# Kernel optimization log

Hardware: AMD Instinct MI355X
Metric: run time of the kernel (lower is better)

## Reference

```python
import jax, jax.numpy as jnp
import numpy as np

B, IN_DIM, NUM_PROD, OUT_DIM = 65536, 1024, 2048, 2048

def setup_inputs() -> dict:
    key = jax.random.key(0)
    k1, k2, k3 = jax.random.split(key, 3)
    x = jax.random.normal(k1, (B, IN_DIM), dtype=jnp.float32)
    prod_indices = jax.random.randint(k2, (NUM_PROD, 2), 0, IN_DIM, dtype=jnp.int32)
    # prod_linear: nn.Linear(num_prod, out_dim, bias=False) -> weight [out_dim, num_prod]
    W_prod = jax.random.normal(k3, (OUT_DIM, NUM_PROD), dtype=jnp.float32) * 0.02
    return {"x": x, "prod_indices": prod_indices, "W_prod": W_prod}

def reference(x, prod_indices, W_prod):
    # calc_quads: for each k, x[..., i_k] * x[..., j_k]  (vectorized gather-multiply)
    # torch loop runs over out_dim == num_prod entries of prod_indices
    quads = x[..., prod_indices[:, 0]] * x[..., prod_indices[:, 1]]  # [B, num_prod]
    # prod_linear (no bias): quads @ W.T
    out = jnp.einsum('bp,op->bo', quads, W_prod)  # [B, out_dim]
    return out
```

## Files before the change

kernel.cpp:

```cpp
#include <hip/hip_runtime.h>
#include <stdint.h>

#define BTOT     65536
#define IN_DIM   1024
#define NUM_PROD 2048
#define OUT_DIM  2048

typedef unsigned short u16;
typedef __attribute__((ext_vector_type(8))) short          bf16x8;
typedef __attribute__((ext_vector_type(8))) unsigned short ushort8;
typedef __attribute__((ext_vector_type(4))) float          f32x4;

__device__ __forceinline__ u16 f2bf(float f) {
    uint32_t u = __float_as_uint(f);
    u = (u + 0x7fff + ((u >> 16) & 1)) >> 16;
    return (u16)u;
}

__device__ __forceinline__ void load_lds16(const void* g, void* l) {
    __builtin_amdgcn_global_load_lds((const __attribute__((address_space(1))) void*)g,
                                     (__attribute__((address_space(3))) void*)l,
                                     16, 0, 0);
}

__global__ __launch_bounds__(256) void cast_w_kernel(const float* __restrict__ W,
                                                     u16* __restrict__ Wb) {
    int i = blockIdx.x * 256 + threadIdx.x;
    const float4* wp = (const float4*)W;
    float4 a = wp[2 * i];
    float4 b = wp[2 * i + 1];
    ushort8 o;
    o[0] = f2bf(a.x); o[1] = f2bf(a.y); o[2] = f2bf(a.z); o[3] = f2bf(a.w);
    o[4] = f2bf(b.x); o[5] = f2bf(b.y); o[6] = f2bf(b.z); o[7] = f2bf(b.w);
    *(ushort8*)(Wb + (size_t)i * 8) = o;
}

#define ROWS_PER_BLOCK 32

__global__ __launch_bounds__(256) void quad_kernel(const float* __restrict__ x,
                                                   const int*   __restrict__ idx,
                                                   u16*         __restrict__ Q,
                                                   int rowBase) {
    __shared__ float xs[IN_DIM];
    const int t = threadIdx.x;

    int2 pr[8];
    const int2* ip = (const int2*)idx;
#pragma unroll
    for (int j = 0; j < 8; ++j) pr[j] = ip[t * 8 + j];

    const int r0 = blockIdx.x * ROWS_PER_BLOCK;
    for (int r = 0; r < ROWS_PER_BLOCK; ++r) {
        const size_t b = (size_t)rowBase + r0 + r;
        __syncthreads();
        ((float4*)xs)[t] = ((const float4*)(x + b * IN_DIM))[t];
        __syncthreads();
        ushort8 o;
#pragma unroll
        for (int j = 0; j < 8; ++j)
            o[j] = f2bf(xs[pr[j].x] * xs[pr[j].y]);
        *(ushort8*)(Q + (size_t)(r0 + r) * NUM_PROD + t * 8) = o;
    }
}

__global__ __launch_bounds__(256) void gemm_bt(const u16* __restrict__ A,
                                               const u16* __restrict__ Bm,
                                               float*     __restrict__ C) {
    __shared__ __align__(16) u16 As[128 * 64];
    __shared__ __align__(16) u16 Bs[128 * 64];

    const int tid  = threadIdx.x;
    const int lane = tid & 63;
    const int wave = tid >> 6;

    const int rowBaseA = blockIdx.y * 128;
    const int colBaseB = blockIdx.x * 128;

    const int wm = (wave >> 1) * 64;
    const int wn = (wave & 1) * 64;
    const int q  = lane >> 4;
    const int lr = lane & 15;

    f32x4 acc[4][4] = {};

    for (int k0 = 0; k0 < NUM_PROD; k0 += 64) {
        __syncthreads();
#pragma unroll
        for (int i = 0; i < 4; ++i) {
            const int physChunkBase = (wave * 4 + i) * 64;
            const int physChunk = physChunkBase + lane;
            const int physRow   = physChunk >> 3;
            const int physCol   = physChunk & 7;
            const int srcChunk  = physCol ^ (physRow & 7);
            load_lds16(A  + (size_t)(rowBaseA + physRow) * NUM_PROD + k0 + srcChunk * 8,
                       &As[physChunkBase * 8]);
            load_lds16(Bm + (size_t)(colBaseB + physRow) * NUM_PROD + k0 + srcChunk * 8,
                       &Bs[physChunkBase * 8]);
        }
        __syncthreads();

#pragma unroll
        for (int ks = 0; ks < 2; ++ks) {
            bf16x8 af[4], bfr[4];
            const int c = ks * 4 + q;
#pragma unroll
            for (int mt = 0; mt < 4; ++mt) {
                const int row = wm + mt * 16 + lr;
                af[mt] = *(const bf16x8*)&As[row * 64 + (c ^ (row & 7)) * 8];
            }
#pragma unroll
            for (int nt = 0; nt < 4; ++nt) {
                const int row = wn + nt * 16 + lr;
                bfr[nt] = *(const bf16x8*)&Bs[row * 64 + (c ^ (row & 7)) * 8];
            }
#pragma unroll
            for (int mt = 0; mt < 4; ++mt)
#pragma unroll
                for (int nt = 0; nt < 4; ++nt)
                    acc[mt][nt] = __builtin_amdgcn_mfma_f32_16x16x32_bf16(
                        af[mt], bfr[nt], acc[mt][nt], 0, 0, 0);
        }
    }

#pragma unroll
    for (int mt = 0; mt < 4; ++mt) {
#pragma unroll
        for (int nt = 0; nt < 4; ++nt) {
            const int col   = colBaseB + wn + nt * 16 + lr;
            const int rbase = rowBaseA + wm + mt * 16 + q * 4;
            float* cp = C + (size_t)rbase * OUT_DIM + col;
#pragma unroll
            for (int r = 0; r < 4; ++r)
                cp[(size_t)r * OUT_DIM] = acc[mt][nt][r];
        }
    }
}

extern "C" void kernel_launch(void* const* d_in, const int* in_sizes, int n_in,
                              void* d_out, int out_size, void* d_ws, size_t ws_size,
                              hipStream_t stream) {
    const float* x   = (const float*)d_in[0];
    const int*   idx = (const int*)d_in[1];
    const float* W   = (const float*)d_in[2];
    float*       out = (float*)d_out;

    const size_t wb_bytes = (size_t)OUT_DIM * NUM_PROD * 2;
    u16* Wb = (u16*)d_ws;
    u16* Q  = (u16*)((char*)d_ws + wb_bytes);

    const size_t qcap = (ws_size > wb_bytes) ? (ws_size - wb_bytes) : 0;
    int rows = BTOT;
    while (rows > 128 && (size_t)rows * NUM_PROD * 2 > qcap) rows >>= 1;

    cast_w_kernel<<<(OUT_DIM * NUM_PROD) / (256 * 8), 256, 0, stream>>>(W, Wb);

    for (int base = 0; base < BTOT; base += rows) {
        quad_kernel<<<rows / ROWS_PER_BLOCK, 256, 0, stream>>>(x, idx, Q, base);
        dim3 g(OUT_DIM / 128, rows / 128);
        gemm_bt<<<g, dim3(256), 0, stream>>>(Q, Wb, out + (size_t)base * OUT_DIM);
    }
}
```

Before: 1.463 ms.

## Rewrite GEMM as pipelined 256x256 tile kernel and per-wave quad producer

Replaces the 128x128 single-buffered GEMM with a 512-thread 256x256 tile kernel. It double-buffers LDS and splits each K step into four sub-tile phases that interleave async global-to-LDS loads with MFMA work, using explicit vmcnt waits, raw barriers and setprio. It also swizzles the block order for L2 reuse. The quad kernel now has each wave own a row, with double-buffered async row prefetch into LDS and a grid-stride loop. The goal is to hide memory latency and raise arithmetic intensity, at the cost of hand-tuned wait counts that are fragile and higher register/LDS pressure.

```diff
diff --git a/kernel.cpp b/kernel.cpp
--- a/kernel.cpp
+++ b/kernel.cpp
@@ -6,6 +6,10 @@
 #define NUM_PROD 2048
 #define OUT_DIM  2048
 
+#define BK        64
+#define NT        (NUM_PROD / BK)
+#define BUF_ELEMS (256 * BK)
+
 typedef unsigned short u16;
 typedef __attribute__((ext_vector_type(8))) short          bf16x8;
 typedef __attribute__((ext_vector_type(8))) unsigned short ushort8;
@@ -22,6 +26,13 @@
                                      (__attribute__((address_space(3))) void*)l,
                                      16, 0, 0);
 }
+
+#define WAITV(n)                                                    \
+    {                                                               \
+        asm volatile("s_waitcnt vmcnt(" #n ")" ::: "memory");       \
+        __builtin_amdgcn_sched_barrier(0);                          \
+    }
+#define FENCE() asm volatile("" ::: "memory")
 
 __global__ __launch_bounds__(256) void cast_w_kernel(const float* __restrict__ W,
                                                      u16* __restrict__ Wb) {
@@ -35,105 +46,189 @@
     *(ushort8*)(Wb + (size_t)i * 8) = o;
 }
 
-#define ROWS_PER_BLOCK 32
-
 __global__ __launch_bounds__(256) void quad_kernel(const float* __restrict__ x,
                                                    const int*   __restrict__ idx,
                                                    u16*         __restrict__ Q,
-                                                   int rowBase) {
-    __shared__ float xs[IN_DIM];
-    const int t = threadIdx.x;
-
-    int2 pr[8];
+                                                   int rowBase, int rowsChunk) {
+    __shared__ float xs[8][IN_DIM];
+    const int lane = threadIdx.x & 63;
+    const int wave = threadIdx.x >> 6;
+    const int gw   = blockIdx.x * 4 + wave;
+    const int NW   = gridDim.x * 4;
+
+    int2 pr[32];
     const int2* ip = (const int2*)idx;
 #pragma unroll
-    for (int j = 0; j < 8; ++j) pr[j] = ip[t * 8 + j];
-
-    const int r0 = blockIdx.x * ROWS_PER_BLOCK;
-    for (int r = 0; r < ROWS_PER_BLOCK; ++r) {
-        const size_t b = (size_t)rowBase + r0 + r;
-        __syncthreads();
-        ((float4*)xs)[t] = ((const float4*)(x + b * IN_DIM))[t];
-        __syncthreads();
-        ushort8 o;
-#pragma unroll
-        for (int j = 0; j < 8; ++j)
-            o[j] = f2bf(xs[pr[j].x] * xs[pr[j].y]);
-        *(ushort8*)(Q + (size_t)(r0 + r) * NUM_PROD + t * 8) = o;
-    }
-}
-
-__global__ __launch_bounds__(256) void gemm_bt(const u16* __restrict__ A,
-                                               const u16* __restrict__ Bm,
-                                               float*     __restrict__ C) {
-    __shared__ __align__(16) u16 As[128 * 64];
-    __shared__ __align__(16) u16 Bs[128 * 64];
+    for (int c = 0; c < 4; ++c)
+#pragma unroll
+        for (int k = 0; k < 8; ++k)
+            pr[c * 8 + k] = ip[(c * 64 + lane) * 8 + k];
+
+    if (gw >= rowsChunk) return;
+
+    {
+        const float* xr = x + (size_t)(rowBase + gw) * IN_DIM;
+        float* slot = xs[wave * 2];
+#pragma unroll
+        for (int i = 0; i < 4; ++i)
+            load_lds16(xr + i * 256 + lane * 4, slot + i * 256);
+    }
+
+    int it = 0;
+    for (int r = gw; r < rowsChunk; r += NW, ++it) {
+        const int rn = r + NW;
+        const bool nxt = (rn < rowsChunk);
+        if (nxt) {
+            const float* xr = x + (size_t)(rowBase + rn) * IN_DIM;
+            float* slot = xs[wave * 2 + ((it + 1) & 1)];
+#pragma unroll
+            for (int i = 0; i < 4; ++i)
+                load_lds16(xr + i * 256 + lane * 4, slot + i * 256);
+        }
+        if (nxt) { if (it) { WAITV(8); } else { WAITV(4); } }
+        else     { if (it) { WAITV(4); } else { WAITV(0); } }
+
+        const float* xr = xs[wave * 2 + (it & 1)];
+        u16* qp = Q + (size_t)r * NUM_PROD;
+#pragma unroll
+        for (int c = 0; c < 4; ++c) {
+            ushort8 o;
+#pragma unroll
+            for (int k = 0; k < 8; ++k) {
+                const int2 p = pr[c * 8 + k];
+                o[k] = f2bf(xr[p.x] * xr[p.y]);
+            }
+            *(ushort8*)(qp + (size_t)(c * 64 + lane) * 8) = o;
+        }
+    }
+}
+
+__device__ __forceinline__ void stage_half(const u16* __restrict__ g, u16* l) {
+    const int lane = threadIdx.x & 63;
+    const int wave = threadIdx.x >> 6;
+#pragma unroll
+    for (int i = 0; i < 2; ++i) {
+        const int chunkBase = i * 512 + wave * 64;
+        const int physChunk = chunkBase + lane;
+        const int physRow   = physChunk >> 3;
+        const int physCol   = physChunk & 7;
+        const int srcChunk  = physCol ^ (physRow & 7);
+        load_lds16(g + (size_t)physRow * NUM_PROD + srcChunk * 8,
+                   l + chunkBase * 8);
+    }
+}
+
+#define PHASE(RH, CH, STAGE_STMT, TAIL_STMT)                                        \
+  {                                                                                 \
+    bf16x8 af[2][4];                                                                \
+    bf16x8 bfr[2][2];                                                               \
+    _Pragma("unroll")                                                               \
+    for (int ks = 0; ks < 2; ++ks) {                                                \
+      _Pragma("unroll")                                                             \
+      for (int mt = 0; mt < 4; ++mt) {                                              \
+        const int rra = (RH) * 128 + wrow + mt * 16 + lr;                           \
+        af[ks][mt] = *(const bf16x8*)&As_t[rra * BK + (((ks * 4 + q) ^ (lr & 7)) * 8)]; \
+      }                                                                             \
+      _Pragma("unroll")                                                             \
+      for (int nt = 0; nt < 2; ++nt) {                                              \
+        const int rrb = (CH) * 128 + wcol + nt * 16 + lr;                           \
+        bfr[ks][nt] = *(const bf16x8*)&Bs_t[rrb * BK + (((ks * 4 + q) ^ (lr & 7)) * 8)]; \
+      }                                                                             \
+    }                                                                               \
+    STAGE_STMT;                                                                     \
+    FENCE();                                                                        \
+    __builtin_amdgcn_s_barrier();                                                   \
+    asm volatile("s_waitcnt lgkmcnt(0)" ::: "memory");                              \
+    __builtin_amdgcn_sched_barrier(0);                                              \
+    __builtin_amdgcn_s_setprio(1);                                                  \
+    _Pragma("unroll")                                                               \
+    for (int ks = 0; ks < 2; ++ks)                                                  \
+      _Pragma("unroll")                                                             \
+      for (int mt = 0; mt < 4; ++mt)                                                \
+        _Pragma("unroll")                                                           \
+        for (int nt = 0; nt < 2; ++nt)                                              \
+          acc[RH][CH][mt][nt] = __builtin_amdgcn_mfma_f32_16x16x32_bf16(            \
+              af[ks][mt], bfr[ks][nt], acc[RH][CH][mt][nt], 0, 0, 0);               \
+    __builtin_amdgcn_s_setprio(0);                                                  \
+    TAIL_STMT;                                                                      \
+    FENCE();                                                                        \
+    __builtin_amdgcn_s_barrier();                                                   \
+  }
+
+__global__ __launch_bounds__(512, 2) void gemm256(const u16* __restrict__ A,
+                                                  const u16* __restrict__ Bm,
+                                                  float*     __restrict__ C) {
+    __shared__ __align__(16) u16 As[2 * BUF_ELEMS];
+    __shared__ __align__(16) u16 Bs[2 * BUF_ELEMS];
 
     const int tid  = threadIdx.x;
     const int lane = tid & 63;
     const int wave = tid >> 6;
-
-    const int rowBaseA = blockIdx.y * 128;
-    const int colBaseB = blockIdx.x * 128;
-
-    const int wm = (wave >> 1) * 64;
-    const int wn = (wave & 1) * 64;
-    const int q  = lane >> 4;
-    const int lr = lane & 15;
-
-    f32x4 acc[4][4] = {};
-
-    for (int k0 = 0; k0 < NUM_PROD; k0 += 64) {
-        __syncthreads();
-#pragma unroll
-        for (int i = 0; i < 4; ++i) {
-            const int physChunkBase = (wave * 4 + i) * 64;
-            const int physChunk = physChunkBase + lane;
-            const int physRow   = physChunk >> 3;
-            const int physCol   = physChunk & 7;
-            const int srcChunk  = physCol ^ (physRow & 7);
-            load_lds16(A  + (size_t)(rowBaseA + physRow) * NUM_PROD + k0 + srcChunk * 8,
-                       &As[physChunkBase * 8]);
-            load_lds16(Bm + (size_t)(colBaseB + physRow) * NUM_PROD + k0 + srcChunk * 8,
-                       &Bs[physChunkBase * 8]);
-        }
-        __syncthreads();
-
-#pragma unroll
-        for (int ks = 0; ks < 2; ++ks) {
-            bf16x8 af[4], bfr[4];
-            const int c = ks * 4 + q;
-#pragma unroll
-            for (int mt = 0; mt < 4; ++mt) {
-                const int row = wm + mt * 16 + lr;
-                af[mt] = *(const bf16x8*)&As[row * 64 + (c ^ (row & 7)) * 8];
-            }
-#pragma unroll
-            for (int nt = 0; nt < 4; ++nt) {
-                const int row = wn + nt * 16 + lr;
-                bfr[nt] = *(const bf16x8*)&Bs[row * 64 + (c ^ (row & 7)) * 8];
-            }
-#pragma unroll
-            for (int mt = 0; mt < 4; ++mt)
-#pragma unroll
-                for (int nt = 0; nt < 4; ++nt)
-                    acc[mt][nt] = __builtin_amdgcn_mfma_f32_16x16x32_bf16(
-                        af[mt], bfr[nt], acc[mt][nt], 0, 0, 0);
-        }
-    }
-
-#pragma unroll
-    for (int mt = 0; mt < 4; ++mt) {
-#pragma unroll
-        for (int nt = 0; nt < 4; ++nt) {
-            const int col   = colBaseB + wn + nt * 16 + lr;
-            const int rbase = rowBaseA + wm + mt * 16 + q * 4;
-            float* cp = C + (size_t)rbase * OUT_DIM + col;
-#pragma unroll
-            for (int r = 0; r < 4; ++r)
-                cp[(size_t)r * OUT_DIM] = acc[mt][nt][r];
-        }
-    }
+    const int q    = lane >> 4;
+    const int lr   = lane & 15;
+    const int wrow = (wave >> 2) * 64;
+    const int wcol = (wave & 3) * 32;
+
+    const int nwg = gridDim.x * gridDim.y;
+    const int bid = blockIdx.y * gridDim.x + blockIdx.x;
+    const int cpx = nwg >> 3;
+    const int swz = (bid & 7) * cpx + (bid >> 3);
+    const int bx  = swz & 7;
+    const int by  = swz >> 3;
+
+    const u16* Ag = A  + (size_t)by * 256 * NUM_PROD;
+    const u16* Bg = Bm + (size_t)bx * 256 * NUM_PROD;
+
+    f32x4 acc[2][2][4][2] = {};
+
+    stage_half(Ag,                           As);
+    stage_half(Bg,                           Bs);
+    stage_half(Bg + (size_t)128 * NUM_PROD,  Bs + 128 * BK);
+    stage_half(Ag + (size_t)128 * NUM_PROD,  As + 128 * BK);
+    stage_half(Ag + BK,                      As + BUF_ELEMS);
+    stage_half(Bg + BK,                      Bs + BUF_ELEMS);
+    WAITV(4);
+    __builtin_amdgcn_s_barrier();
+
+    for (int t = 0; t < NT; ++t) {
+        const u16* As_t = As + (t & 1) * BUF_ELEMS;
+        const u16* Bs_t = Bs + (t & 1) * BUF_ELEMS;
+        u16* As_n = As + ((t + 1) & 1) * BUF_ELEMS;
+        u16* Bs_n = Bs + ((t + 1) & 1) * BUF_ELEMS;
+        u16* As_c = As + (t & 1) * BUF_ELEMS;
+        u16* Bs_c = Bs + (t & 1) * BUF_ELEMS;
+        const int tn = t + 1, tnn = t + 2;
+
+        PHASE(0, 0,
+              { if (tn < NT) stage_half(Bg + (size_t)128 * NUM_PROD + tn * BK, Bs_n + 128 * BK); },
+              { })
+        PHASE(0, 1,
+              { if (tn < NT) stage_half(Ag + (size_t)128 * NUM_PROD + tn * BK, As_n + 128 * BK); },
+              { })
+        PHASE(1, 0,
+              { if (tnn < NT) stage_half(Ag + (size_t)tnn * BK, As_c); },
+              { })
+        PHASE(1, 1,
+              { if (tnn < NT) stage_half(Bg + (size_t)tnn * BK, Bs_c); },
+              { if (tnn < NT) { WAITV(4); } else if (tn < NT) { WAITV(0); } })
+    }
+
+    float* Cb = C + (size_t)by * 256 * OUT_DIM + (size_t)bx * 256;
+#pragma unroll
+    for (int rh = 0; rh < 2; ++rh)
+#pragma unroll
+      for (int ch = 0; ch < 2; ++ch)
+#pragma unroll
+        for (int mt = 0; mt < 4; ++mt)
+#pragma unroll
+          for (int nt = 0; nt < 2; ++nt) {
+            const int row0 = rh * 128 + wrow + mt * 16 + q * 4;
+            const int col  = ch * 128 + wcol + nt * 16 + lr;
+            float* cp = Cb + (size_t)row0 * OUT_DIM + col;
+#pragma unroll
+            for (int rr = 0; rr < 4; ++rr)
+                cp[(size_t)rr * OUT_DIM] = acc[rh][ch][mt][nt][rr];
+          }
 }
 
 extern "C" void kernel_launch(void* const* d_in, const int* in_sizes, int n_in,
@@ -150,13 +245,13 @@
 
     const size_t qcap = (ws_size > wb_bytes) ? (ws_size - wb_bytes) : 0;
     int rows = BTOT;
-    while (rows > 128 && (size_t)rows * NUM_PROD * 2 > qcap) rows >>= 1;
+    while (rows > 256 && (size_t)rows * NUM_PROD * 2 > qcap) rows >>= 1;
 
     cast_w_kernel<<<(OUT_DIM * NUM_PROD) / (256 * 8), 256, 0, stream>>>(W, Wb);
 
     for (int base = 0; base < BTOT; base += rows) {
-        quad_kernel<<<rows / ROWS_PER_BLOCK, 256, 0, stream>>>(x, idx, Q, base);
-        dim3 g(OUT_DIM / 128, rows / 128);
-        gemm_bt<<<g, dim3(256), 0, stream>>>(Q, Wb, out + (size_t)base * OUT_DIM);
-    }
-}
+        quad_kernel<<<rows / 32, 256, 0, stream>>>(x, idx, Q, base, rows);
+        dim3 g(OUT_DIM / 256, rows / 256);
+        gemm256<<<g, dim3(512), 0, stream>>>(Q, Wb, out + (size_t)base * OUT_DIM);
+    }
+}
```

Result: faster. 1.338 ms (-8.6%).
